# Kernel optimization log

Measured on AMD Instinct MI355X. Metric: run time of the kernel, lower is better.

Reference implementation:

```python
import jax, jax.numpy as jnp
import numpy as np

N = 50000
E = 800000
D = 128          # node_dim
ED = 64          # edge_dim
H = 4            # n_heads
HD = D // H      # head_dim
LN_EPS = 1e-5


def setup_inputs() -> dict:
    key = jax.random.key(0)
    ks = jax.random.split(key, 10)
    s = 0.05
    return {
        "x": jax.random.normal(ks[0], (N, D), dtype=jnp.float32),
        "edge_index": jax.random.randint(ks[1], (2, E), 0, N, dtype=jnp.int32),
        "edge_attr": jax.random.normal(ks[2], (E, ED), dtype=jnp.float32),
        # parameters (torch Linear transposed to [in, out])
        "align_w": jax.random.normal(ks[3], (2 * D + ED, H), dtype=jnp.float32) * s,
        "align_b": jnp.zeros((H,), dtype=jnp.float32),
        "value_w": jax.random.normal(ks[4], (D, D), dtype=jnp.float32) * s,
        "value_b": jnp.zeros((D,), dtype=jnp.float32),
        "proj_w": jax.random.normal(ks[5], (D, D), dtype=jnp.float32) * s,
        "proj_b": jnp.zeros((D,), dtype=jnp.float32),
        "ln_g": jnp.ones((D,), dtype=jnp.float32),
        "ln_b": jnp.zeros((D,), dtype=jnp.float32),
    }


def reference(x, edge_index, edge_attr, align_w, align_b, value_w, value_b,
              proj_w, proj_b, ln_g, ln_b):
    row, col = edge_index[0], edge_index[1]          # [E], [E]
    h_i = x[row]                                     # [E, D] gather (dst)
    h_j = x[col]                                     # [E, D] gather (src)
    cat_feat = jnp.concatenate([h_i, h_j, edge_attr], axis=-1)  # [E, 2D+ED]
    scores = cat_feat @ align_w + align_b            # [E, H]

    # numerically-stable segment softmax over incoming edges of each dst node
    max_per_node = jax.ops.segment_max(scores, row, num_segments=N)  # [N, H]
    scores_exp = jnp.exp(scores - max_per_node[row])                 # [E, H]
    sum_exp = jax.ops.segment_sum(scores_exp, row, num_segments=N)   # [N, H]
    alpha = scores_exp / (sum_exp[row] + 1e-8)                       # [E, H]

    V = (h_j @ value_w + value_b).reshape(E, H, HD)                  # [E, H, HD]
    weighted = (V * alpha[:, :, None]).reshape(E, D)                 # [E, D]
    context = jax.ops.segment_sum(weighted, row, num_segments=N)     # [N, D]

    y = x + context @ proj_w + proj_b                                # [N, D]
    mu = jnp.mean(y, axis=-1, keepdims=True)
    var = jnp.mean((y - mu) ** 2, axis=-1, keepdims=True)
    return (y - mu) / jnp.sqrt(var + LN_EPS) * ln_g + ln_b
```

## Files before the change

kernel.cpp:

```cpp
#include <hip/hip_runtime.h>
#include <hip/hip_bf16.h>
#include <math.h>

#define N_NODES 50000
#define N_EDGES 800000
#define DIM 128
#define EDIM 64
#define NH 4
#define DEG_CAP 64

__global__ __launch_bounds__(256) void k_bucket(
    const int* __restrict__ ei, int* cnt, int2* __restrict__ ecolid) {
    int e = blockIdx.x * 256 + threadIdx.x;
    if (e < N_EDGES) {
        int row = ei[e], col = ei[N_EDGES + e];
        int pos = atomicAdd(&cnt[row], 1);
        if (pos < DEG_CAP) ecolid[(size_t)row * DEG_CAP + pos] = make_int2(col, e);
    }
}

__global__ __launch_bounds__(128) void k_node_pre(
    const float* __restrict__ x, const float* __restrict__ vw, const float* __restrict__ vb,
    const float* __restrict__ aw,
    unsigned int* __restrict__ Vxb,
    float* __restrict__ a_src) {
    __shared__ float xs[32][129];
    int t = threadIdx.x;
    int nb = blockIdx.x * 32;
    #pragma unroll
    for (int i = 0; i < 8; ++i) {
        int idx = i * 128 + t;
        int m = idx >> 5, k4 = idx & 31;
        int n = nb + m;
        float4 v = make_float4(0.f, 0.f, 0.f, 0.f);
        if (n < N_NODES) v = *(const float4*)(x + (size_t)n * DIM + k4 * 4);
        xs[m][k4*4+0] = v.x; xs[m][k4*4+1] = v.y; xs[m][k4*4+2] = v.z; xs[m][k4*4+3] = v.w;
    }
    __syncthreads();
    int c = t & 31, mg = t >> 5;
    int d0 = c * 4, m0 = mg * 8;
    float acc[8][4];
    #pragma unroll
    for (int j = 0; j < 8; ++j) { acc[j][0]=0.f; acc[j][1]=0.f; acc[j][2]=0.f; acc[j][3]=0.f; }
    for (int k = 0; k < DIM; ++k) {
        float4 w = *(const float4*)(vw + (size_t)k * DIM + d0);
        #pragma unroll
        for (int j = 0; j < 8; ++j) {
            float xv = xs[m0 + j][k];
            acc[j][0] += xv * w.x; acc[j][1] += xv * w.y;
            acc[j][2] += xv * w.z; acc[j][3] += xv * w.w;
        }
    }
    float4 vb4 = *(const float4*)(vb + d0);
    #pragma unroll
    for (int j = 0; j < 8; ++j) {
        int n = nb + m0 + j;
        if (n < N_NODES) {
            __hip_bfloat162 p0 = __float22bfloat162_rn(
                make_float2(acc[j][0]+vb4.x, acc[j][1]+vb4.y));
            __hip_bfloat162 p1 = __float22bfloat162_rn(
                make_float2(acc[j][2]+vb4.z, acc[j][3]+vb4.w));
            uint2 u;
            u.x = *reinterpret_cast<unsigned int*>(&p0);
            u.y = *reinterpret_cast<unsigned int*>(&p1);
            *(uint2*)(Vxb + (size_t)n * 64 + c * 2) = u;
        }
    }
    {
        int m = t >> 2, h = t & 3;
        float s = 0.f;
        for (int k = 0; k < DIM; ++k) s += xs[m][k] * aw[(size_t)(DIM + k) * NH + h];
        int n = nb + m;
        if (n < N_NODES) a_src[(size_t)n * NH + h] = s;
    }
}

__global__ __launch_bounds__(256) void k_mega(
    const int* __restrict__ cnt, const int2* __restrict__ ecolid,
    const float* __restrict__ ea, const float* __restrict__ aw,
    const float* __restrict__ a_src, const unsigned int* __restrict__ Vxb,
    const float* __restrict__ x, const float* __restrict__ pw,
    const float* __restrict__ pb, const float* __restrict__ lg,
    const float* __restrict__ lb, float* __restrict__ out) {
    __shared__ float cs[16][130];
    int t = threadIdx.x;
    int lane = t & 63, w = t >> 6;
    int nb = blockIdx.x * 16;
    int l = lane & 15, grp = lane >> 4;
    int hd = l >> 2;
    float wreg[16];
    #pragma unroll
    for (int j = 0; j < 4; ++j)
        #pragma unroll
        for (int h = 0; h < NH; ++h)
            wreg[j * 4 + h] = aw[1024 + (l * 4 + j) * 4 + h];
    for (int jj = 0; jj < 4; ++jj) {
        int m = w * 4 + jj;
        int n = nb + m;
        int deg = cnt[n]; deg = deg < DEG_CAP ? deg : DEG_CAP;
        int2 ce = (lane < deg) ? ecolid[(size_t)n * DEG_CAP + lane] : make_int2(0, 0);
        int colv = ce.x, eidv = ce.y;
        float a0=0.f,a1=0.f,a2=0.f,a3=0.f,a4=0.f,a5=0.f,a6=0.f,a7=0.f,sw=0.f;
        int jm4 = (deg + 3) & ~3;
        #pragma unroll 4
        for (int j = grp; j < jm4; j += 4) {
            int col = __shfl(colv, j);
            int eid = __shfl(eidv, j);
            float4 v = *(const float4*)(ea + (size_t)eid * EDIM + l * 4);
            float p0 = v.x*wreg[0] + v.y*wreg[4] + v.z*wreg[8]  + v.w*wreg[12];
            float p1 = v.x*wreg[1] + v.y*wreg[5] + v.z*wreg[9]  + v.w*wreg[13];
            float p2 = v.x*wreg[2] + v.y*wreg[6] + v.z*wreg[10] + v.w*wreg[14];
            float p3 = v.x*wreg[3] + v.y*wreg[7] + v.z*wreg[11] + v.w*wreg[15];
            #pragma unroll
            for (int off = 1; off < 16; off <<= 1) {
                p0 += __shfl_xor(p0, off);
                p1 += __shfl_xor(p1, off);
                p2 += __shfl_xor(p2, off);
                p3 += __shfl_xor(p3, off);
            }
            float ph = (hd == 0) ? p0 : (hd == 1) ? p1 : (hd == 2) ? p2 : p3;
            float s = ph + a_src[(size_t)col * NH + hd];
            float wgt = (j < deg) ? __expf(s) : 0.f;
            uint4 u = *(const uint4*)(Vxb + (size_t)col * 64 + l * 4);
            float f0 = __uint_as_float(u.x << 16), f1 = __uint_as_float(u.x & 0xffff0000u);
            float f2 = __uint_as_float(u.y << 16), f3 = __uint_as_float(u.y & 0xffff0000u);
            float f4 = __uint_as_float(u.z << 16), f5 = __uint_as_float(u.z & 0xffff0000u);
            float f6 = __uint_as_float(u.w << 16), f7 = __uint_as_float(u.w & 0xffff0000u);
            a0 += f0*wgt; a1 += f1*wgt; a2 += f2*wgt; a3 += f3*wgt;
            a4 += f4*wgt; a5 += f5*wgt; a6 += f6*wgt; a7 += f7*wgt;
            sw += wgt;
        }
        #pragma unroll
        for (int off = 16; off < 64; off <<= 1) {
            a0 += __shfl_xor(a0, off); a1 += __shfl_xor(a1, off);
            a2 += __shfl_xor(a2, off); a3 += __shfl_xor(a3, off);
            a4 += __shfl_xor(a4, off); a5 += __shfl_xor(a5, off);
            a6 += __shfl_xor(a6, off); a7 += __shfl_xor(a7, off);
            sw += __shfl_xor(sw, off);
        }
        if (lane < 16) {
            float inv = 1.0f / (sw + 1e-8f);
            int d = l * 8;
            cs[m][d+0] = a0*inv; cs[m][d+1] = a1*inv;
            cs[m][d+2] = a2*inv; cs[m][d+3] = a3*inv;
            cs[m][d+4] = a4*inv; cs[m][d+5] = a5*inv;
            cs[m][d+6] = a6*inv; cs[m][d+7] = a7*inv;
        }
    }
    __syncthreads();
    int d0 = (t & 63) * 2, mg = t >> 6;
    int m0 = mg * 4;
    float acc[4][2];
    #pragma unroll
    for (int j = 0; j < 4; ++j) { acc[j][0] = 0.f; acc[j][1] = 0.f; }
    for (int k = 0; k < DIM; ++k) {
        float2 wv = *(const float2*)(pw + (size_t)k * DIM + d0);
        #pragma unroll
        for (int j = 0; j < 4; ++j) {
            float cv = cs[m0 + j][k];
            acc[j][0] += cv * wv.x; acc[j][1] += cv * wv.y;
        }
    }
    float2 pb2 = *(const float2*)(pb + d0);
    float2 g2  = *(const float2*)(lg + d0);
    float2 b2  = *(const float2*)(lb + d0);
    #pragma unroll
    for (int j = 0; j < 4; ++j) {
        int n = nb + m0 + j;
        float2 xv = *(const float2*)(x + (size_t)n * DIM + d0);
        float y0 = xv.x + acc[j][0] + pb2.x;
        float y1 = xv.y + acc[j][1] + pb2.y;
        float ps = y0 + y1, pq = y0*y0 + y1*y1;
        #pragma unroll
        for (int off = 1; off < 64; off <<= 1) {
            ps += __shfl_xor(ps, off);
            pq += __shfl_xor(pq, off);
        }
        float mu = ps * (1.0f / DIM);
        float var = pq * (1.0f / DIM) - mu * mu;
        float rstd = rsqrtf(var + 1e-5f);
        float2 o;
        o.x = (y0 - mu) * rstd * g2.x + b2.x;
        o.y = (y1 - mu) * rstd * g2.y + b2.y;
        *(float2*)(out + (size_t)n * DIM + d0) = o;
    }
}

extern "C" void kernel_launch(void* const* d_in, const int* in_sizes, int n_in,
                              void* d_out, int out_size, void* d_ws, size_t ws_size,
                              hipStream_t stream) {
    const float* x       = (const float*)d_in[0];
    const int*   ei      = (const int*)  d_in[1];
    const float* ea      = (const float*)d_in[2];
    const float* align_w = (const float*)d_in[3];
    const float* value_w = (const float*)d_in[5];
    const float* value_b = (const float*)d_in[6];
    const float* proj_w  = (const float*)d_in[7];
    const float* proj_b  = (const float*)d_in[8];
    const float* ln_g    = (const float*)d_in[9];
    const float* ln_b    = (const float*)d_in[10];
    float* out = (float*)d_out;
    float* ws  = (float*)d_ws;

    unsigned int* Vxb = (unsigned int*)ws;
    float* a_src   = ws + 3200000;
    int2*  ecolid  = (int2*)(ws + 3400000);
    int*   cnt     = (int*)(ws + 9800000);

    hipMemsetAsync(cnt, 0, (size_t)N_NODES * sizeof(int), stream);
    k_bucket<<<(N_EDGES + 255) / 256, 256, 0, stream>>>(ei, cnt, ecolid);
    k_node_pre<<<(N_NODES + 31) / 32, 128, 0, stream>>>(
        x, value_w, value_b, align_w, Vxb, a_src);
    k_mega<<<N_NODES / 16, 256, 0, stream>>>(
        cnt, ecolid, ea, align_w, a_src, Vxb, x, proj_w, proj_b, ln_g, ln_b, out);
}
```

Measured before the change: 237.7 us.

## Merge bucket and node-pre kernels; one node per wave in mega kernel

Fuses the edge-bucketing and node-precompute kernels into one launch whose block index picks the role, so both run at the same time and a launch is saved. The precompute uses 256 threads with 4 rows each. The mega kernel now gives each wave a single node (4 nodes per block, 4x more blocks). Its projection GEMM is split over k across waves with a shared-memory reduction, and the edge score reduction uses a transpose-style shuffle with fewer shuffles. This adds parallelism and latency hiding at the cost of more blocks and more shared-memory traffic, and it reloads the projection weights more often per node.

After: 233.5 us. About the same (-1.8%).

```diff
diff --git a/kernel.cpp b/kernel.cpp
--- a/kernel.cpp
+++ b/kernel.cpp
@@ -8,28 +8,29 @@
 #define EDIM 64
 #define NH 4
 #define DEG_CAP 64
-
-__global__ __launch_bounds__(256) void k_bucket(
-    const int* __restrict__ ei, int* cnt, int2* __restrict__ ecolid) {
-    int e = blockIdx.x * 256 + threadIdx.x;
-    if (e < N_EDGES) {
-        int row = ei[e], col = ei[N_EDGES + e];
-        int pos = atomicAdd(&cnt[row], 1);
-        if (pos < DEG_CAP) ecolid[(size_t)row * DEG_CAP + pos] = make_int2(col, e);
-    }
-}
-
-__global__ __launch_bounds__(128) void k_node_pre(
-    const float* __restrict__ x, const float* __restrict__ vw, const float* __restrict__ vb,
-    const float* __restrict__ aw,
-    unsigned int* __restrict__ Vxb,
-    float* __restrict__ a_src) {
+#define BKT_BLOCKS 3125
+#define PRE_BLOCKS 1563
+
+__global__ __launch_bounds__(256) void k_prep(
+    const int* __restrict__ ei, int* cnt, int2* __restrict__ ecolid,
+    const float* __restrict__ x, const float* __restrict__ vw,
+    const float* __restrict__ vb, const float* __restrict__ aw,
+    unsigned int* __restrict__ Vxb, float* __restrict__ a_src) {
     __shared__ float xs[32][129];
     int t = threadIdx.x;
-    int nb = blockIdx.x * 32;
-    #pragma unroll
-    for (int i = 0; i < 8; ++i) {
-        int idx = i * 128 + t;
+    if (blockIdx.x < BKT_BLOCKS) {
+        int e = blockIdx.x * 256 + t;
+        if (e < N_EDGES) {
+            int row = ei[e], col = ei[N_EDGES + e];
+            int pos = atomicAdd(&cnt[row], 1);
+            if (pos < DEG_CAP) ecolid[(size_t)row * DEG_CAP + pos] = make_int2(col, e);
+        }
+        return;
+    }
+    int nb = (blockIdx.x - BKT_BLOCKS) * 32;
+    #pragma unroll
+    for (int i = 0; i < 4; ++i) {
+        int idx = i * 256 + t;
         int m = idx >> 5, k4 = idx & 31;
         int n = nb + m;
         float4 v = make_float4(0.f, 0.f, 0.f, 0.f);
@@ -38,14 +39,14 @@
     }
     __syncthreads();
     int c = t & 31, mg = t >> 5;
-    int d0 = c * 4, m0 = mg * 8;
-    float acc[8][4];
-    #pragma unroll
-    for (int j = 0; j < 8; ++j) { acc[j][0]=0.f; acc[j][1]=0.f; acc[j][2]=0.f; acc[j][3]=0.f; }
+    int d0 = c * 4, m0 = mg * 4;
+    float acc[4][4];
+    #pragma unroll
+    for (int j = 0; j < 4; ++j) { acc[j][0]=0.f; acc[j][1]=0.f; acc[j][2]=0.f; acc[j][3]=0.f; }
     for (int k = 0; k < DIM; ++k) {
         float4 w = *(const float4*)(vw + (size_t)k * DIM + d0);
         #pragma unroll
-        for (int j = 0; j < 8; ++j) {
+        for (int j = 0; j < 4; ++j) {
             float xv = xs[m0 + j][k];
             acc[j][0] += xv * w.x; acc[j][1] += xv * w.y;
             acc[j][2] += xv * w.z; acc[j][3] += xv * w.w;
@@ -53,7 +54,7 @@
     }
     float4 vb4 = *(const float4*)(vb + d0);
     #pragma unroll
-    for (int j = 0; j < 8; ++j) {
+    for (int j = 0; j < 4; ++j) {
         int n = nb + m0 + j;
         if (n < N_NODES) {
             __hip_bfloat162 p0 = __float22bfloat162_rn(
@@ -66,7 +67,7 @@
             *(uint2*)(Vxb + (size_t)n * 64 + c * 2) = u;
         }
     }
-    {
+    if (t < 128) {
         int m = t >> 2, h = t & 3;
         float s = 0.f;
         for (int k = 0; k < DIM; ++k) s += xs[m][k] * aw[(size_t)(DIM + k) * NH + h];
@@ -82,94 +83,105 @@
     const float* __restrict__ x, const float* __restrict__ pw,
     const float* __restrict__ pb, const float* __restrict__ lg,
     const float* __restrict__ lb, float* __restrict__ out) {
-    __shared__ float cs[16][130];
+    __shared__ float cs[4][130];
+    __shared__ float red[4][4][128];
     int t = threadIdx.x;
     int lane = t & 63, w = t >> 6;
-    int nb = blockIdx.x * 16;
+    int nb = blockIdx.x * 4;
+    int n = nb + w;
     int l = lane & 15, grp = lane >> 4;
     int hd = l >> 2;
+    int trl = (lane & 48) | ((l & 3) << 2) | (l >> 2);
     float wreg[16];
     #pragma unroll
     for (int j = 0; j < 4; ++j)
         #pragma unroll
         for (int h = 0; h < NH; ++h)
             wreg[j * 4 + h] = aw[1024 + (l * 4 + j) * 4 + h];
-    for (int jj = 0; jj < 4; ++jj) {
-        int m = w * 4 + jj;
-        int n = nb + m;
-        int deg = cnt[n]; deg = deg < DEG_CAP ? deg : DEG_CAP;
-        int2 ce = (lane < deg) ? ecolid[(size_t)n * DEG_CAP + lane] : make_int2(0, 0);
-        int colv = ce.x, eidv = ce.y;
-        float a0=0.f,a1=0.f,a2=0.f,a3=0.f,a4=0.f,a5=0.f,a6=0.f,a7=0.f,sw=0.f;
-        int jm4 = (deg + 3) & ~3;
-        #pragma unroll 4
-        for (int j = grp; j < jm4; j += 4) {
-            int col = __shfl(colv, j);
-            int eid = __shfl(eidv, j);
-            float4 v = *(const float4*)(ea + (size_t)eid * EDIM + l * 4);
-            float p0 = v.x*wreg[0] + v.y*wreg[4] + v.z*wreg[8]  + v.w*wreg[12];
-            float p1 = v.x*wreg[1] + v.y*wreg[5] + v.z*wreg[9]  + v.w*wreg[13];
-            float p2 = v.x*wreg[2] + v.y*wreg[6] + v.z*wreg[10] + v.w*wreg[14];
-            float p3 = v.x*wreg[3] + v.y*wreg[7] + v.z*wreg[11] + v.w*wreg[15];
+    int deg = cnt[n]; deg = deg < DEG_CAP ? deg : DEG_CAP;
+    int2 ce = (lane < deg) ? ecolid[(size_t)n * DEG_CAP + lane] : make_int2(0, 0);
+    int colv = ce.x, eidv = ce.y;
+    float a0=0.f,a1=0.f,a2=0.f,a3=0.f,a4=0.f,a5=0.f,a6=0.f,a7=0.f,sw=0.f;
+    int jm4 = (deg + 3) & ~3;
+    #pragma unroll 4
+    for (int j = grp; j < jm4; j += 4) {
+        int col = __shfl(colv, j);
+        int eid = __shfl(eidv, j);
+        float4 v = *(const float4*)(ea + (size_t)eid * EDIM + l * 4);
+        float p0 = v.x*wreg[0] + v.y*wreg[4] + v.z*wreg[8]  + v.w*wreg[12];
+        float p1 = v.x*wreg[1] + v.y*wreg[5] + v.z*wreg[9]  + v.w*wreg[13];
+        float p2 = v.x*wreg[2] + v.y*wreg[6] + v.z*wreg[10] + v.w*wreg[14];
+        float p3 = v.x*wreg[3] + v.y*wreg[7] + v.z*wreg[11] + v.w*wreg[15];
+        #pragma unroll
+        for (int off = 1; off < 4; off <<= 1) {
+            p0 += __shfl_xor(p0, off);
+            p1 += __shfl_xor(p1, off);
+            p2 += __shfl_xor(p2, off);
+            p3 += __shfl_xor(p3, off);
+        }
+        int r = l & 3;
+        float pr = (r == 0) ? p0 : (r == 1) ? p1 : (r == 2) ? p2 : p3;
+        pr += __shfl_xor(pr, 4);
+        pr += __shfl_xor(pr, 8);
+        float ph = __shfl(pr, trl);
+        float s = ph + a_src[(size_t)col * NH + hd];
+        float wgt = (j < deg) ? __expf(s) : 0.f;
+        uint4 u = *(const uint4*)(Vxb + (size_t)col * 64 + l * 4);
+        float f0 = __uint_as_float(u.x << 16), f1 = __uint_as_float(u.x & 0xffff0000u);
+        float f2 = __uint_as_float(u.y << 16), f3 = __uint_as_float(u.y & 0xffff0000u);
+        float f4 = __uint_as_float(u.z << 16), f5 = __uint_as_float(u.z & 0xffff0000u);
+        float f6 = __uint_as_float(u.w << 16), f7 = __uint_as_float(u.w & 0xffff0000u);
+        a0 += f0*wgt; a1 += f1*wgt; a2 += f2*wgt; a3 += f3*wgt;
+        a4 += f4*wgt; a5 += f5*wgt; a6 += f6*wgt; a7 += f7*wgt;
+        sw += wgt;
+    }
+    #pragma unroll
+    for (int off = 16; off < 64; off <<= 1) {
+        a0 += __shfl_xor(a0, off); a1 += __shfl_xor(a1, off);
+        a2 += __shfl_xor(a2, off); a3 += __shfl_xor(a3, off);
+        a4 += __shfl_xor(a4, off); a5 += __shfl_xor(a5, off);
+        a6 += __shfl_xor(a6, off); a7 += __shfl_xor(a7, off);
+        sw += __shfl_xor(sw, off);
+    }
+    if (lane < 16) {
+        float inv = 1.0f / (sw + 1e-8f);
+        int d = l * 8;
+        cs[w][d+0] = a0*inv; cs[w][d+1] = a1*inv;
+        cs[w][d+2] = a2*inv; cs[w][d+3] = a3*inv;
+        cs[w][d+4] = a4*inv; cs[w][d+5] = a5*inv;
+        cs[w][d+6] = a6*inv; cs[w][d+7] = a7*inv;
+    }
+    __syncthreads();
+    {
+        int d0 = lane * 2;
+        float ac[4][2];
+        #pragma unroll
+        for (int j = 0; j < 4; ++j) { ac[j][0] = 0.f; ac[j][1] = 0.f; }
+        int k0 = w * 32;
+        for (int k = k0; k < k0 + 32; ++k) {
+            float2 wv = *(const float2*)(pw + (size_t)k * DIM + d0);
             #pragma unroll
-            for (int off = 1; off < 16; off <<= 1) {
-                p0 += __shfl_xor(p0, off);
-                p1 += __shfl_xor(p1, off);
-                p2 += __shfl_xor(p2, off);
-                p3 += __shfl_xor(p3, off);
+            for (int j = 0; j < 4; ++j) {
+                float cv = cs[j][k];
+                ac[j][0] += cv * wv.x; ac[j][1] += cv * wv.y;
             }
-            float ph = (hd == 0) ? p0 : (hd == 1) ? p1 : (hd == 2) ? p2 : p3;
-            float s = ph + a_src[(size_t)col * NH + hd];
-            float wgt = (j < deg) ? __expf(s) : 0.f;
-            uint4 u = *(const uint4*)(Vxb + (size_t)col * 64 + l * 4);
-            float f0 = __uint_as_float(u.x << 16), f1 = __uint_as_float(u.x & 0xffff0000u);
-            float f2 = __uint_as_float(u.y << 16), f3 = __uint_as_float(u.y & 0xffff0000u);
-            float f4 = __uint_as_float(u.z << 16), f5 = __uint_as_float(u.z & 0xffff0000u);
-            float f6 = __uint_as_float(u.w << 16), f7 = __uint_as_float(u.w & 0xffff0000u);
-            a0 += f0*wgt; a1 += f1*wgt; a2 += f2*wgt; a3 += f3*wgt;
-            a4 += f4*wgt; a5 += f5*wgt; a6 += f6*wgt; a7 += f7*wgt;
-            sw += wgt;
-        }
-        #pragma unroll
-        for (int off = 16; off < 64; off <<= 1) {
-            a0 += __shfl_xor(a0, off); a1 += __shfl_xor(a1, off);
-            a2 += __shfl_xor(a2, off); a3 += __shfl_xor(a3, off);
-            a4 += __shfl_xor(a4, off); a5 += __shfl_xor(a5, off);
-            a6 += __shfl_xor(a6, off); a7 += __shfl_xor(a7, off);
-            sw += __shfl_xor(sw, off);
-        }
-        if (lane < 16) {
-            float inv = 1.0f / (sw + 1e-8f);
-            int d = l * 8;
-            cs[m][d+0] = a0*inv; cs[m][d+1] = a1*inv;
-            cs[m][d+2] = a2*inv; cs[m][d+3] = a3*inv;
-            cs[m][d+4] = a4*inv; cs[m][d+5] = a5*inv;
-            cs[m][d+6] = a6*inv; cs[m][d+7] = a7*inv;
+        }
+        #pragma unroll
+        for (int j = 0; j < 4; ++j) {
+            red[w][j][d0]     = ac[j][0];
+            red[w][j][d0 + 1] = ac[j][1];
         }
     }
     __syncthreads();
-    int d0 = (t & 63) * 2, mg = t >> 6;
-    int m0 = mg * 4;
-    float acc[4][2];
-    #pragma unroll
-    for (int j = 0; j < 4; ++j) { acc[j][0] = 0.f; acc[j][1] = 0.f; }
-    for (int k = 0; k < DIM; ++k) {
-        float2 wv = *(const float2*)(pw + (size_t)k * DIM + d0);
-        #pragma unroll
-        for (int j = 0; j < 4; ++j) {
-            float cv = cs[m0 + j][k];
-            acc[j][0] += cv * wv.x; acc[j][1] += cv * wv.y;
-        }
-    }
-    float2 pb2 = *(const float2*)(pb + d0);
-    float2 g2  = *(const float2*)(lg + d0);
-    float2 b2  = *(const float2*)(lb + d0);
-    #pragma unroll
-    for (int j = 0; j < 4; ++j) {
-        int n = nb + m0 + j;
-        float2 xv = *(const float2*)(x + (size_t)n * DIM + d0);
-        float y0 = xv.x + acc[j][0] + pb2.x;
-        float y1 = xv.y + acc[j][1] + pb2.y;
+    {
+        int jj = w;
+        int dd = lane, d0 = dd * 2;
+        float y0 = red[0][jj][d0] + red[1][jj][d0] + red[2][jj][d0] + red[3][jj][d0];
+        float y1 = red[0][jj][d0+1] + red[1][jj][d0+1] + red[2][jj][d0+1] + red[3][jj][d0+1];
+        float2 pb2 = *(const float2*)(pb + d0);
+        float2 xv  = *(const float2*)(x + (size_t)n * DIM + d0);
+        y0 += xv.x + pb2.x;
+        y1 += xv.y + pb2.y;
         float ps = y0 + y1, pq = y0*y0 + y1*y1;
         #pragma unroll
         for (int off = 1; off < 64; off <<= 1) {
@@ -179,6 +191,8 @@
         float mu = ps * (1.0f / DIM);
         float var = pq * (1.0f / DIM) - mu * mu;
         float rstd = rsqrtf(var + 1e-5f);
+        float2 g2 = *(const float2*)(lg + d0);
+        float2 b2 = *(const float2*)(lb + d0);
         float2 o;
         o.x = (y0 - mu) * rstd * g2.x + b2.x;
         o.y = (y1 - mu) * rstd * g2.y + b2.y;
@@ -208,9 +222,8 @@
     int*   cnt     = (int*)(ws + 9800000);
 
     hipMemsetAsync(cnt, 0, (size_t)N_NODES * sizeof(int), stream);
-    k_bucket<<<(N_EDGES + 255) / 256, 256, 0, stream>>>(ei, cnt, ecolid);
-    k_node_pre<<<(N_NODES + 31) / 32, 128, 0, stream>>>(
-        x, value_w, value_b, align_w, Vxb, a_src);
-    k_mega<<<N_NODES / 16, 256, 0, stream>>>(
+    k_prep<<<BKT_BLOCKS + PRE_BLOCKS, 256, 0, stream>>>(
+        ei, cnt, ecolid, x, value_w, value_b, align_w, Vxb, a_src);
+    k_mega<<<N_NODES / 4, 256, 0, stream>>>(
         cnt, ecolid, ea, align_w, a_src, Vxb, x, proj_w, proj_b, ln_g, ln_b, out);
 }
```
